# Performance work log

Hardware: AMD Instinct MI355X
Metric: run time of the kernel (lower is better)

Reference implementation:

```python
import jax, jax.numpy as jnp
import numpy as np

LEAKAGE = 0.9
RADIUS = 0.1
AVG_DEGREE = 6


def setup_inputs() -> dict:
    key = jax.random.key(0)
    k1, k2, k3, k4, k5 = jax.random.split(key, 5)
    B, T, I, N, O = 16, 2048, 32, 2048, 32
    input_sequence = jax.random.normal(k1, (B, T, I), dtype=jnp.float32)
    # sparse reservoir matrix, uniform(-1,1) with density avg_degree/N, scaled to spectral radius
    A = jax.random.uniform(k2, (N, N), minval=-1.0, maxval=1.0, dtype=jnp.float32)
    mask = jax.random.uniform(k3, (N, N)) < (AVG_DEGREE / N)
    A = jnp.where(mask, A, 0.0)
    # approximate spectral normalization (power-iteration-free surrogate scale)
    A = A * (RADIUS / jnp.max(jnp.abs(jnp.linalg.eigvals(A))).astype(jnp.float32))
    Win = (RADIUS) * (2.0 * jax.random.uniform(k4, (N, I), dtype=jnp.float32) - 1.0)
    Wout_w = jax.random.normal(k5, (O, N), dtype=jnp.float32) / np.sqrt(N)
    return {"input_sequence": input_sequence, "Win": Win, "A": A, "Wout_w": Wout_w, "washout_len": 64}


def reference(input_sequence, Win, A, Wout_w, washout_len):
    # input projection for all timesteps at once (noise_std = 0.0)
    inp = jnp.einsum('bti,ni->btn', input_sequence, Win)  # [B, T, N]
    B = input_sequence.shape[0]
    N = A.shape[0]
    h0 = jnp.zeros((B, N), dtype=input_sequence.dtype)
    At = A.T

    def step(h, u_t):
        # h: [B, N], u_t: [B, N]
        h_new = (1.0 - LEAKAGE) * h + LEAKAGE * jnp.tanh(h @ At + u_t)
        return h_new, h_new

    _, hs = jax.lax.scan(step, h0, jnp.swapaxes(inp, 0, 1))  # hs: [T, B, N]
    hs = jnp.swapaxes(hs, 0, 1)  # [B, T, N]
    h_list = hs[:, washout_len - 1:]  # keep steps i >= washout_len - 1
    return jnp.einsum('btn,on->bto', h_list, Wout_w)
```

## Files before the change

kernel.cpp:

```cpp
#include <hip/hip_runtime.h>
#include <stdint.h>

#define BB 16
#define TT 2048
#define NI 32
#define NN 2048
#define NO 32
#define WASH 64
#define TO (TT - WASH + 1)
#define W 24
#define WT 24
#define CH 16
#define HBST 2056
#define HBROW 4112
#define UROWB 4132
#define U2OFF 65792
#define LDS_BYTES (U2OFF + CH*UROWB)

typedef short bfvec __attribute__((ext_vector_type(8)));
typedef float f4_t  __attribute__((ext_vector_type(4)));

__device__ inline unsigned short f2bf(float f) {
  unsigned int u = __builtin_bit_cast(unsigned int, f);
  unsigned int r = u + 0x7fffu + ((u >> 16) & 1u);
  return (unsigned short)(r >> 16);
}
__device__ inline float bf2f(unsigned short s) {
  unsigned int u = ((unsigned int)s) << 16;
  return __builtin_bit_cast(float, u);
}
__device__ inline float tanh_fast(float x) {
  x = fminf(15.f, fmaxf(-15.f, x));
  float e = __expf(x + x);
  float r = __builtin_amdgcn_rcpf(e + 1.0f);
  return (e - 1.0f) * r;
}

__global__ void build_ell(const float* __restrict__ A, uint32_t* __restrict__ ell,
                          uint32_t* __restrict__ deg) {
  int gw = (int)((blockIdx.x * blockDim.x + threadIdx.x) >> 6);
  int lane = (int)(threadIdx.x & 63);
  if (gw >= NN) return;
  const float* row = A + (size_t)gw * NN;
  int base = 0;
  for (int c = 0; c < NN; c += 64) {
    float v = row[c + lane];
    bool nz = (v != 0.0f);
    unsigned long long mask = __ballot(nz);
    int pre = __popcll(mask & ((1ull << lane) - 1ull));
    if (nz) {
      int idx = base + pre;
      if (idx < W) {
        uint32_t packed = (((uint32_t)f2bf(v)) << 16) | (uint32_t)((c + lane) * 4);
        ell[(size_t)gw * W + idx] = packed;
      }
    }
    base += __popcll(mask);
  }
  int d = base < W ? base : W;
  if (lane == 0) deg[gw] = (uint32_t)d;
  for (int k = d + lane; k < W; k += 64) ell[(size_t)gw * W + k] = 0u;
}

__global__ void sortperm(const uint32_t* __restrict__ deg, uint32_t* __restrict__ perm,
                         uint32_t* __restrict__ invp) {
  __shared__ int dg[NN];
  int tid = (int)threadIdx.x;
  for (int i = tid; i < NN; i += 256) dg[i] = (int)deg[i];
  __syncthreads();
  int r = (int)blockIdx.x * 256 + tid;
  int d = dg[r];
  int rank = 0;
  for (int j = 0; j < NN; ++j) {
    int dj = dg[j];
    rank += (dj < d) || (dj == d && j < r);
  }
  perm[rank] = (uint32_t)r;
  invp[r] = (uint32_t)rank;
}

__global__ void pairsort(const uint32_t* __restrict__ deg, const uint32_t* __restrict__ perm,
                         uint32_t* __restrict__ pairrank, uint32_t* __restrict__ pp) {
  __shared__ int ps[1024];
  int tid = (int)threadIdx.x;
  for (int i = tid; i < 1024; i += 256) {
    int d0 = (int)deg[perm[i]]; if (d0 > W) d0 = W;
    int d1 = (int)deg[perm[2047 - i]]; if (d1 > W) d1 = W;
    int s = d0 + d1; if (s > WT) s = WT;
    ps[i] = s;
  }
  __syncthreads();
  int p = (int)blockIdx.x * 256 + tid;
  int s = ps[p];
  int rank = 0;
  for (int j = 0; j < 1024; ++j) {
    int sj = ps[j];
    rank += (sj < s) || (sj == s && j < p);
  }
  pairrank[p] = (uint32_t)rank;
  pp[rank] = (uint32_t)p;
}

__device__ inline int rank2pos(int r, const uint32_t* pairrank) {
  return (r < 1024) ? (2 * (int)pairrank[r]) : (2 * (int)pairrank[2047 - r] + 1);
}

__device__ inline int bcnt_get(unsigned long long lo, unsigned long long hi, int b) {
  return (int)(((b < 16) ? (lo >> (4 * b)) : (hi >> (4 * (b - 16)))) & 15ull);
}

__global__ void build_pairs(const uint32_t* __restrict__ ell, const uint32_t* __restrict__ deg,
                            const uint32_t* __restrict__ perm, const uint32_t* __restrict__ invp,
                            const uint32_t* __restrict__ pairrank, const uint32_t* __restrict__ pp,
                            uint32_t* __restrict__ pa, uint32_t* __restrict__ pva,
                            uint32_t* __restrict__ pvb, uint32_t* __restrict__ wavecnt) {
  int blk = (int)blockIdx.x;
  int lane = (int)threadIdx.x;
  int t = blk * 64 + lane;
  int p = (int)pp[t];
  uint32_t a_[WT], u_[WT], w_[WT];
  int cnt = 0;
  {
    int ro = (int)perm[p];
    int d = (int)deg[ro]; if (d > W) d = W;
    for (int k = 0; k < d && cnt < WT; ++k) {
      uint32_t e = ell[(size_t)ro * W + k];
      int pos = rank2pos((int)invp[(e & 0xffffu) >> 2], pairrank);
      a_[cnt] = (uint32_t)(pos * 2);
      u_[cnt] = e & 0xffff0000u;
      w_[cnt] = 0u;
      ++cnt;
    }
    ro = (int)perm[2047 - p];
    d = (int)deg[ro]; if (d > W) d = W;
    for (int k = 0; k < d && cnt < WT; ++k) {
      uint32_t e = ell[(size_t)ro * W + k];
      int pos = rank2pos((int)invp[(e & 0xffffu) >> 2], pairrank);
      a_[cnt] = (uint32_t)(pos * 2);
      u_[cnt] = 0u;
      w_[cnt] = e & 0xffff0000u;
      ++cnt;
    }
  }
  int m = cnt;
  #pragma unroll
  for (int off = 32; off; off >>= 1) m = max(m, __shfl_xor(m, off));
  int S = m < 8 ? 8 : (m > 24 ? 24 : m);
  if (lane == 0) wavecnt[blk] = (uint32_t)S;

  uint32_t sa[WT], su[WT], sw[WT];
  for (int s = 0; s < WT; ++s) {
    sa[s] = ((uint32_t)((lane + s) & 31)) << 2;
    su[s] = 0u; sw[s] = 0u;
  }
  uint32_t used = 0;
  for (int s = 0; s < S; ++s) {
    unsigned long long clo = 0ull, chi = 0ull;
    bool placed = false;
    for (int round = 0; round < 6; ++round) {
      bool force = (round == 5);
      int best = -1, bestc = 999;
      if (!placed) {
        for (int k = 0; k < WT; ++k) {
          if (k >= cnt) break;
          if ((used >> k) & 1u) continue;
        int b = (int)((a_[k] >> 2) & 31u);
          int c = bcnt_get(clo, chi, b);
          if (c < bestc) { bestc = c; best = k; }
        }
      }
      int pb = (!placed && best >= 0) ? (int)((a_[best] >> 2) & 31u) : 32;
      int shift = (s * 19 + round * 7) & 63;
      int mypos = (lane - shift) & 63;
      for (int b = 0; b < 32; ++b) {
        unsigned long long mb = __ballot(pb == b);
        if (!mb) continue;
        unsigned long long mbr = (mb >> shift) | (mb << ((64 - shift) & 63));
        int have = bcnt_get(clo, chi, b);
        int cap = 2 - have; if (cap < 0) cap = 0;
        if (pb == b) {
          int rank = (int)__popcll(mbr & ((1ull << (unsigned)mypos) - 1ull));
          if (force || rank < cap) {
            placed = true;
            used |= (1u << (unsigned)best);
            sa[s] = a_[best]; su[s] = u_[best]; sw[s] = w_[best];
          }
        }
        int nprop = (int)__popcll(mb);
        int add = force ? nprop : (nprop < cap ? nprop : cap);
        int room = 15 - have; if (add > room) add = room;
        if (add > 0) {
          if (b < 16) clo += ((unsigned long long)add) << (4 * b);
          else        chi += ((unsigned long long)add) << (4 * (b - 16));
        }
      }
    }
    if (!placed) {
      int pick = lane & 31;
      for (int j = 0; j < 32; ++j) {
        int b = (lane + j) & 31;
        if (bcnt_get(clo, chi, b) < 2) { pick = b; break; }
      }
      sa[s] = ((uint32_t)pick) << 2;
    }
  }
  for (int k = 0; k < WT; ++k) {
    pa[(size_t)t * WT + k] = sa[k];
    pva[(size_t)t * WT + k] = su[k];
    pvb[(size_t)t * WT + k] = sw[k];
  }
}

__global__ void build_frags(const float* __restrict__ Win, const float* __restrict__ Wout,
                            const uint32_t* __restrict__ perm, const uint32_t* __restrict__ pp,
                            uint32_t* __restrict__ winf, uint32_t* __restrict__ woutf) {
  int f = (int)(blockIdx.x * blockDim.x + threadIdx.x);
  if (f < 32768) {
    int reg = f & 3, lane = (f >> 2) & 63, ntg = f >> 8;
    int n = (ntg << 4) + (lane & 15);
    int k = ((lane >> 4) << 3) + reg * 2;
    int p = (int)pp[n >> 1];
    int np = (int)perm[(n & 1) ? (2047 - p) : p];
    uint32_t lo = f2bf(Win[(size_t)np * NI + k]);
    uint32_t hi = f2bf(Win[(size_t)np * NI + k + 1]);
    winf[f] = lo | (hi << 16);
  } else {
    int g = f - 32768;
    int reg = g & 3, lane = (g >> 2) & 63, kt = (g >> 8) & 63, ot = g >> 14;
    int o = (ot << 4) + (lane & 15);
    int n = (kt << 5) + ((lane >> 4) << 3) + reg * 2;
    int p = (int)pp[n >> 1];
    int n0 = (int)perm[p];
    int n1 = (int)perm[2047 - p];
    uint32_t lo = f2bf(Wout[(size_t)o * NN + n0]);
    uint32_t hi = f2bf(Wout[(size_t)o * NN + n1]);
    woutf[g] = lo | (hi << 16);
  }
}

#define ENT(K, BASE)                                                                 \
  {                                                                                  \
    float hv = bf2f(*(const unsigned short*)(smem + (BASE) + ea##K));                \
    y0 = __builtin_fmaf(__builtin_bit_cast(float, va##K), hv, y0);                   \
    y1 = __builtin_fmaf(__builtin_bit_cast(float, vb##K), hv, y1);                   \
  }

#define ENTS8(B)  ENT(0,B) ENT(1,B) ENT(2,B) ENT(3,B) ENT(4,B) ENT(5,B) ENT(6,B) ENT(7,B)
#define ENTS9(B)  ENTS8(B)  ENT(8,B)
#define ENTS10(B) ENTS9(B)  ENT(9,B)
#define ENTS11(B) ENTS10(B) ENT(10,B)
#define ENTS12(B) ENTS11(B) ENT(11,B)
#define ENTS13(B) ENTS12(B) ENT(12,B)
#define ENTS14(B) ENTS13(B) ENT(13,B)
#define ENTS15(B) ENTS14(B) ENT(14,B)
#define ENTS16(B) ENTS15(B) ENT(15,B)
#define ENTS17(B) ENTS16(B) ENT(16,B)
#define ENTS18(B) ENTS17(B) ENT(17,B)
#define ENTS19(B) ENTS18(B) ENT(18,B)
#define ENTS20(B) ENTS19(B) ENT(19,B)
#define ENTS21(B) ENTS20(B) ENT(20,B)
#define ENTS22(B) ENTS21(B) ENT(21,B)
#define ENTS23(B) ENTS22(B) ENT(22,B)
#define ENTS24(B) ENTS23(B) ENT(23,B)

#define STEPLOOP(ENTS)                                                               \
  _Pragma("unroll 1")                                                                \
  for (int tt = 0; tt < CH; ++tt) {                                                  \
    const int po = ((tt + CH - 1) & (CH - 1)) * HBROW;                               \
    uint32_t uw = *(const uint32_t*)(smem + u2a + tt * UROWB);                       \
    float y0 = bf2f((unsigned short)(uw & 0xffffu));                                 \
    float y1 = bf2f((unsigned short)(uw >> 16));                                     \
    ENTS(po)                                                                         \
    float hn0 = 0.1f * h0 + 0.9f * tanh_fast(y0);                                    \
    float hn1 = 0.1f * h1 + 0.9f * tanh_fast(y1);                                    \
    *(uint32_t*)(smem + hwa + tt * HBROW) =                                          \
        (uint32_t)f2bf(hn0) | ((uint32_t)f2bf(hn1) << 16);                           \
    h0 = hn0; h1 = hn1;                                                              \
    __syncthreads();                                                                 \
  }

__global__ __launch_bounds__(1024, 1) void rec_kernel(
    const float* __restrict__ x,
    const uint32_t* __restrict__ pa, const uint32_t* __restrict__ pva,
    const uint32_t* __restrict__ pvb, const uint32_t* __restrict__ wavecnt,
    const uint32_t* __restrict__ winf, const uint32_t* __restrict__ woutf,
    float* __restrict__ out) {
  extern __shared__ char smem[];
  unsigned short* hb = (unsigned short*)smem;
  float* oscratch = (float*)(smem + U2OFF);

  const int tid = (int)threadIdx.x;
  const int b = (int)blockIdx.x;
  const int lane = tid & 63;
  const int wv = tid >> 6;
  const int la15 = lane & 15;
  const int lg = lane >> 4;
  const int u2a = U2OFF + (tid << 2);
  const int hwa = tid << 2;

  int cnt = __builtin_amdgcn_readfirstlane((int)wavecnt[wv]);

  uint32_t ea0, ea1, ea2, ea3, ea4, ea5, ea6, ea7, ea8, ea9, ea10, ea11,
           ea12, ea13, ea14, ea15, ea16, ea17, ea18, ea19, ea20, ea21, ea22, ea23;
  uint32_t va0, va1, va2, va3, va4, va5, va6, va7, va8, va9, va10, va11,
           va12, va13, va14, va15, va16, va17, va18, va19, va20, va21, va22, va23;
  uint32_t vb0, vb1, vb2, vb3, vb4, vb5, vb6, vb7, vb8, vb9, vb10, vb11,
           vb12, vb13, vb14, vb15, vb16, vb17, vb18, vb19, vb20, vb21, vb22, vb23;
  {
    const uint4* qa = (const uint4*)(pa + (size_t)tid * WT);
    const uint4* qv = (const uint4*)(pva + (size_t)tid * WT);
    const uint4* qw = (const uint4*)(pvb + (size_t)tid * WT);
    uint4 A0 = qa[0], A1 = qa[1], A2 = qa[2], A3 = qa[3], A4 = qa[4], A5 = qa[5];
    uint4 V0 = qv[0], V1 = qv[1], V2 = qv[2], V3 = qv[3], V4 = qv[4], V5 = qv[5];
    uint4 B0 = qw[0], B1 = qw[1], B2 = qw[2], B3 = qw[3], B4 = qw[4], B5 = qw[5];
    ea0 = A0.x; ea1 = A0.y; ea2 = A0.z; ea3 = A0.w;
    ea4 = A1.x; ea5 = A1.y; ea6 = A1.z; ea7 = A1.w;
    ea8 = A2.x; ea9 = A2.y; ea10 = A2.z; ea11 = A2.w;
    ea12 = A3.x; ea13 = A3.y; ea14 = A3.z; ea15 = A3.w;
    ea16 = A4.x; ea17 = A4.y; ea18 = A4.z; ea19 = A4.w;
    ea20 = A5.x; ea21 = A5.y; ea22 = A5.z; ea23 = A5.w;
    va0 = V0.x; va1 = V0.y; va2 = V0.z; va3 = V0.w;
    va4 = V1.x; va5 = V1.y; va6 = V1.z; va7 = V1.w;
    va8 = V2.x; va9 = V2.y; va10 = V2.z; va11 = V2.w;
    va12 = V3.x; va13 = V3.y; va14 = V3.z; va15 = V3.w;
    va16 = V4.x; va17 = V4.y; va18 = V4.z; va19 = V4.w;
    va20 = V5.x; va21 = V5.y; va22 = V5.z; va23 = V5.w;
    vb0 = B0.x; vb1 = B0.y; vb2 = B0.z; vb3 = B0.w;
    vb4 = B1.x; vb5 = B1.y; vb6 = B1.z; vb7 = B1.w;
    vb8 = B2.x; vb9 = B2.y; vb10 = B2.z; vb11 = B2.w;
    vb12 = B3.x; vb13 = B3.y; vb14 = B3.z; vb15 = B3.w;
    vb16 = B4.x; vb17 = B4.y; vb18 = B4.z; vb19 = B4.w;
    vb20 = B5.x; vb21 = B5.y; vb22 = B5.z; vb23 = B5.w;
  }

  *(uint32_t*)(smem + (CH - 1) * HBROW + (tid << 2)) = 0u;
  float h0 = 0.0f, h1 = 0.0f;

  for (int c = 0; c < TT / CH; ++c) {
    const int t0 = c * CH;

    {
      const float* xp = x + ((size_t)b * TT + (t0 + la15)) * NI + (lg << 3);
      float4 x0 = *(const float4*)xp;
      float4 x1 = *(const float4*)(xp + 4);
      union { unsigned short u16[8]; bfvec v; } af;
      af.u16[0]=f2bf(x0.x); af.u16[1]=f2bf(x0.y); af.u16[2]=f2bf(x0.z); af.u16[3]=f2bf(x0.w);
      af.u16[4]=f2bf(x1.x); af.u16[5]=f2bf(x1.y); af.u16[6]=f2bf(x1.z); af.u16[7]=f2bf(x1.w);
      #pragma unroll
      for (int nt = 0; nt < 8; ++nt) {
        int ntg = (wv << 3) + nt;
        union { uint4 q; bfvec v; } bw;
        bw.q = *(const uint4*)(winf + (((size_t)ntg * 64 + lane) << 2));
        f4_t acc = {0.f, 0.f, 0.f, 0.f};
        acc = __builtin_amdgcn_mfma_f32_16x16x32_bf16(bw.v, af.v, acc, 0, 0, 0);
        int dw = (ntg << 3) + (lg << 1);
        uint32_t w0 = (uint32_t)f2bf(acc[0]) | ((uint32_t)f2bf(acc[1]) << 16);
        uint32_t w1 = (uint32_t)f2bf(acc[2]) | ((uint32_t)f2bf(acc[3]) << 16);
        char* ub = smem + U2OFF + la15 * UROWB + (dw << 2);
        *(uint32_t*)(ub) = w0;
        *(uint32_t*)(ub + 4) = w1;
      }
    }
    __syncthreads();

    asm volatile("" : "+s"(cnt));
    if      (cnt <= 8)  { STEPLOOP(ENTS8)  }
    else if (cnt == 9)  { STEPLOOP(ENTS9)  }
    else if (cnt == 10) { STEPLOOP(ENTS10) }
    else if (cnt == 11) { STEPLOOP(ENTS11) }
    else if (cnt == 12) { STEPLOOP(ENTS12) }
    else if (cnt == 13) { STEPLOOP(ENTS13) }
    else if (cnt == 14) { STEPLOOP(ENTS14) }
    else if (cnt == 15) { STEPLOOP(ENTS15) }
    else if (cnt == 16) { STEPLOOP(ENTS16) }
    else if (cnt == 17) { STEPLOOP(ENTS17) }
    else if (cnt == 18) { STEPLOOP(ENTS18) }
    else if (cnt == 19) { STEPLOOP(ENTS19) }
    else if (cnt == 20) { STEPLOOP(ENTS20) }
    else if (cnt == 21) { STEPLOOP(ENTS21) }
    else if (cnt == 22) { STEPLOOP(ENTS22) }
    else if (cnt == 23) { STEPLOOP(ENTS23) }
    else                { STEPLOOP(ENTS24) }

    {
      f4_t oa0 = {0.f,0.f,0.f,0.f}, oa1 = {0.f,0.f,0.f,0.f};
      #pragma unroll
      for (int k4 = 0; k4 < 4; ++k4) {
        int kt = (wv << 2) + k4;
        union { uint4 q; bfvec v; } ha, w0, w1;
        ha.q = *(const uint4*)(hb + (size_t)la15 * HBST + (kt << 5) + (lg << 3));
        w0.q = *(const uint4*)(woutf + (((size_t)(kt) * 64 + lane) << 2));
        w1.q = *(const uint4*)(woutf + (((size_t)(64 + kt) * 64 + lane) << 2));
        oa0 = __builtin_amdgcn_mfma_f32_16x16x32_bf16(ha.v, w0.v, oa0, 0, 0, 0);
        oa1 = __builtin_amdgcn_mfma_f32_16x16x32_bf16(ha.v, w1.v, oa1, 0, 0, 0);
      }
      float* os = oscratch + (wv << 9);
      int tb = lg << 2;
      #pragma unroll
      for (int r = 0; r < 4; ++r) os[(tb + r) * 32 + la15] = oa0[r];
      #pragma unroll
      for (int r = 0; r < 4; ++r) os[(tb + r) * 32 + 16 + la15] = oa1[r];
    }
    __syncthreads();
    if (tid < 512) {
      float s = 0.0f;
      #pragma unroll
      for (int w2 = 0; w2 < 16; ++w2) s += oscratch[(w2 << 9) + tid];
      int tg = t0 + (tid >> 5);
      if (tg >= WASH - 1)
        out[((size_t)b * TO + (tg - (WASH - 1))) * NO + (tid & 31)] = s;
    }
    __syncthreads();
  }
}

extern "C" void kernel_launch(void* const* d_in, const int* in_sizes, int n_in,
                              void* d_out, int out_size, void* d_ws, size_t ws_size,
                              hipStream_t stream) {
  (void)in_sizes; (void)n_in; (void)out_size; (void)ws_size;
  const float* x    = (const float*)d_in[0];
  const float* Win  = (const float*)d_in[1];
  const float* A    = (const float*)d_in[2];
  const float* Wout = (const float*)d_in[3];
  float* out = (float*)d_out;

  char* ws = (char*)d_ws;
  uint32_t* ell      = (uint32_t*)(ws);
  uint32_t* deg      = (uint32_t*)(ws + 196608);
  uint32_t* perm     = (uint32_t*)(ws + 204800);
  uint32_t* invp     = (uint32_t*)(ws + 212992);
  uint32_t* pairrank = (uint32_t*)(ws + 221184);
  uint32_t* pp       = (uint32_t*)(ws + 225280);
  uint32_t* wavecnt  = (uint32_t*)(ws + 229376);
  uint32_t* pa       = (uint32_t*)(ws + 229504);
  uint32_t* pva      = (uint32_t*)(ws + 327808);
  uint32_t* pvb      = (uint32_t*)(ws + 426112);
  uint32_t* winf     = (uint32_t*)(ws + 524416);
  uint32_t* woutf    = (uint32_t*)(ws + 655488);

  hipFuncSetAttribute((const void*)rec_kernel,
                      hipFuncAttributeMaxDynamicSharedMemorySize, 160 * 1024);

  hipLaunchKernelGGL(build_ell, dim3(512), dim3(256), 0, stream, A, ell, deg);
  hipLaunchKernelGGL(sortperm, dim3(8), dim3(256), 0, stream, deg, perm, invp);
  hipLaunchKernelGGL(pairsort, dim3(4), dim3(256), 0, stream, deg, perm, pairrank, pp);
  hipLaunchKernelGGL(build_pairs, dim3(16), dim3(64), 0, stream,
                     ell, deg, perm, invp, pairrank, pp, pa, pva, pvb, wavecnt);
  hipLaunchKernelGGL(build_frags, dim3(256), dim3(256), 0, stream, Win, Wout, perm, pp, winf, woutf);
  hipLaunchKernelGGL(rec_kernel, dim3(16), dim3(1024), LDS_BYTES, stream,
                     x, pa, pva, pvb, wavecnt, winf, woutf, out);
}
```

Measured before the change: 2.858 ms.

## Duplicate hidden state into a swizzled LDS copy to cut bank conflicts

Each step now writes the new hidden state twice: once to the existing history buffer and once to a second, swizzled double-buffered copy. Even-indexed gather entries read from the original layout and odd-indexed ones from the swizzled copy. The host-side slot assignment is rewritten to place one entry per free bank in each half-wave, choosing between the two layouts. This aims to cut LDS bank conflicts in the sparse gather, at the cost of an extra LDS store per step and a larger LDS footprint. The row padding is also removed.

```diff
diff --git a/kernel.cpp b/kernel.cpp
--- a/kernel.cpp
+++ b/kernel.cpp
@@ -11,11 +11,12 @@
 #define W 24
 #define WT 24
 #define CH 16
-#define HBST 2056
-#define HBROW 4112
+#define HBST 2048
+#define HBROW 4096
 #define UROWB 4132
-#define U2OFF 65792
-#define LDS_BYTES (U2OFF + CH*UROWB)
+#define U2OFF 65536
+#define C1OFF 131712
+#define LDS_BYTES (C1OFF + 8192)
 
 typedef short bfvec __attribute__((ext_vector_type(8)));
 typedef float f4_t  __attribute__((ext_vector_type(4)));
@@ -105,8 +106,9 @@
   return (r < 1024) ? (2 * (int)pairrank[r]) : (2 * (int)pairrank[2047 - r] + 1);
 }
 
-__device__ inline int bcnt_get(unsigned long long lo, unsigned long long hi, int b) {
-  return (int)(((b < 16) ? (lo >> (4 * b)) : (hi >> (4 * (b - 16)))) & 15ull);
+__device__ inline int c1pos(int t) {
+  int l = t & 31, h = t >> 5;
+  return (h << 5) | ((17 * l + 5 * h) & 31);
 }
 
 __global__ void build_pairs(const uint32_t* __restrict__ ell, const uint32_t* __restrict__ deg,
@@ -116,9 +118,10 @@
                             uint32_t* __restrict__ pvb, uint32_t* __restrict__ wavecnt) {
   int blk = (int)blockIdx.x;
   int lane = (int)threadIdx.x;
+  int half = lane >> 5;
   int t = blk * 64 + lane;
   int p = (int)pp[t];
-  uint32_t a_[WT], u_[WT], w_[WT];
+  uint32_t a0_[WT], a1_[WT], u_[WT], w_[WT];
   int cnt = 0;
   {
     int ro = (int)perm[p];
@@ -126,7 +129,8 @@
     for (int k = 0; k < d && cnt < WT; ++k) {
       uint32_t e = ell[(size_t)ro * W + k];
       int pos = rank2pos((int)invp[(e & 0xffffu) >> 2], pairrank);
-      a_[cnt] = (uint32_t)(pos * 2);
+      a0_[cnt] = (uint32_t)(pos * 2);
+      a1_[cnt] = (uint32_t)(c1pos(pos >> 1) * 4 + (pos & 1) * 2);
       u_[cnt] = e & 0xffff0000u;
       w_[cnt] = 0u;
       ++cnt;
@@ -136,7 +140,8 @@
     for (int k = 0; k < d && cnt < WT; ++k) {
       uint32_t e = ell[(size_t)ro * W + k];
       int pos = rank2pos((int)invp[(e & 0xffffu) >> 2], pairrank);
-      a_[cnt] = (uint32_t)(pos * 2);
+      a0_[cnt] = (uint32_t)(pos * 2);
+      a1_[cnt] = (uint32_t)(c1pos(pos >> 1) * 4 + (pos & 1) * 2);
       u_[cnt] = 0u;
       w_[cnt] = e & 0xffff0000u;
       ++cnt;
@@ -154,52 +159,64 @@
     su[s] = 0u; sw[s] = 0u;
   }
   uint32_t used = 0;
+  int rem = cnt;
   for (int s = 0; s < S; ++s) {
-    unsigned long long clo = 0ull, chi = 0ull;
+    int copy = s & 1;
+    unsigned long long occ = 0ull;
     bool placed = false;
-    for (int round = 0; round < 6; ++round) {
-      bool force = (round == 5);
-      int best = -1, bestc = 999;
-      if (!placed) {
+    const int R = 4;
+    for (int r = 0; r < R; ++r) {
+      bool last = (r == R - 1);
+      bool urgent = (rem >= S - s);
+      int pk = -1, pb = 32;
+      if (!placed && rem > 0) {
         for (int k = 0; k < WT; ++k) {
           if (k >= cnt) break;
           if ((used >> k) & 1u) continue;
-        int b = (int)((a_[k] >> 2) & 31u);
-          int c = bcnt_get(clo, chi, b);
-          if (c < bestc) { bestc = c; best = k; }
+          int b = copy ? (int)((a1_[k] >> 2) & 31u) : (int)((a0_[k] >> 2) & 31u);
+          if (!((occ >> (half * 32 + b)) & 1ull)) { pk = k; pb = b; break; }
         }
-      }
-      int pb = (!placed && best >= 0) ? (int)((a_[best] >> 2) & 31u) : 32;
-      int shift = (s * 19 + round * 7) & 63;
-      int mypos = (lane - shift) & 63;
+        if (pk < 0 && last && urgent) {
+          for (int k = 0; k < WT; ++k) {
+            if (k >= cnt) break;
+            if (!((used >> k) & 1u)) {
+              pk = k;
+              pb = copy ? (int)((a1_[k] >> 2) & 31u) : (int)((a0_[k] >> 2) & 31u);
+              break;
+            }
+          }
+        }
+      }
+      int shift = (s * 19 + r * 7) & 31;
       for (int b = 0; b < 32; ++b) {
         unsigned long long mb = __ballot(pb == b);
         if (!mb) continue;
-        unsigned long long mbr = (mb >> shift) | (mb << ((64 - shift) & 63));
-        int have = bcnt_get(clo, chi, b);
-        int cap = 2 - have; if (cap < 0) cap = 0;
-        if (pb == b) {
-          int rank = (int)__popcll(mbr & ((1ull << (unsigned)mypos) - 1ull));
-          if (force || rank < cap) {
-            placed = true;
-            used |= (1u << (unsigned)best);
-            sa[s] = a_[best]; su[s] = u_[best]; sw[s] = w_[best];
+        for (int h = 0; h < 2; ++h) {
+          uint32_t mh = (uint32_t)(mb >> (h * 32));
+          if (!mh) continue;
+          bool freeb = !((occ >> (h * 32 + b)) & 1ull);
+          uint32_t mhr = (mh >> shift) | (mh << ((32 - shift) & 31));
+          int winpos = __ffs(mhr) - 1;
+          int winlane = ((winpos + shift) & 31) + h * 32;
+          if (freeb) occ |= 1ull << (h * 32 + b);
+          if (pb == b && half == h && !placed) {
+            bool win = (lane == winlane);
+            if ((freeb && win) || (last && urgent)) {
+              placed = true;
+              used |= 1u << (unsigned)pk;
+              sa[s] = copy ? a1_[pk] : a0_[pk];
+              su[s] = u_[pk]; sw[s] = w_[pk];
+              rem--;
+            }
           }
         }
-        int nprop = (int)__popcll(mb);
-        int add = force ? nprop : (nprop < cap ? nprop : cap);
-        int room = 15 - have; if (add > room) add = room;
-        if (add > 0) {
-          if (b < 16) clo += ((unsigned long long)add) << (4 * b);
-          else        chi += ((unsigned long long)add) << (4 * (b - 16));
-        }
       }
     }
     if (!placed) {
-      int pick = lane & 31;
+      int pick = (lane + s) & 31;
       for (int j = 0; j < 32; ++j) {
-        int b = (lane + j) & 31;
-        if (bcnt_get(clo, chi, b) < 2) { pick = b; break; }
+        int b = (lane + s + j) & 31;
+        if (!((occ >> (half * 32 + b)) & 1ull)) { pick = b; break; }
       }
       sa[s] = ((uint32_t)pick) << 2;
     }
@@ -238,43 +255,45 @@
   }
 }
 
-#define ENT(K, BASE)                                                                 \
+#define ENT(K)                                                                       \
   {                                                                                  \
-    float hv = bf2f(*(const unsigned short*)(smem + (BASE) + ea##K));                \
+    float hv = bf2f(*(const unsigned short*)(smem + ((((K) & 1) ? po1 : po0)) + ea##K)); \
     y0 = __builtin_fmaf(__builtin_bit_cast(float, va##K), hv, y0);                   \
     y1 = __builtin_fmaf(__builtin_bit_cast(float, vb##K), hv, y1);                   \
   }
 
-#define ENTS8(B)  ENT(0,B) ENT(1,B) ENT(2,B) ENT(3,B) ENT(4,B) ENT(5,B) ENT(6,B) ENT(7,B)
-#define ENTS9(B)  ENTS8(B)  ENT(8,B)
-#define ENTS10(B) ENTS9(B)  ENT(9,B)
-#define ENTS11(B) ENTS10(B) ENT(10,B)
-#define ENTS12(B) ENTS11(B) ENT(11,B)
-#define ENTS13(B) ENTS12(B) ENT(12,B)
-#define ENTS14(B) ENTS13(B) ENT(13,B)
-#define ENTS15(B) ENTS14(B) ENT(14,B)
-#define ENTS16(B) ENTS15(B) ENT(15,B)
-#define ENTS17(B) ENTS16(B) ENT(16,B)
-#define ENTS18(B) ENTS17(B) ENT(17,B)
-#define ENTS19(B) ENTS18(B) ENT(18,B)
-#define ENTS20(B) ENTS19(B) ENT(19,B)
-#define ENTS21(B) ENTS20(B) ENT(20,B)
-#define ENTS22(B) ENTS21(B) ENT(21,B)
-#define ENTS23(B) ENTS22(B) ENT(22,B)
-#define ENTS24(B) ENTS23(B) ENT(23,B)
+#define ENTS8  ENT(0) ENT(1) ENT(2) ENT(3) ENT(4) ENT(5) ENT(6) ENT(7)
+#define ENTS9  ENTS8  ENT(8)
+#define ENTS10 ENTS9  ENT(9)
+#define ENTS11 ENTS10 ENT(10)
+#define ENTS12 ENTS11 ENT(11)
+#define ENTS13 ENTS12 ENT(12)
+#define ENTS14 ENTS13 ENT(13)
+#define ENTS15 ENTS14 ENT(14)
+#define ENTS16 ENTS15 ENT(15)
+#define ENTS17 ENTS16 ENT(16)
+#define ENTS18 ENTS17 ENT(17)
+#define ENTS19 ENTS18 ENT(18)
+#define ENTS20 ENTS19 ENT(19)
+#define ENTS21 ENTS20 ENT(20)
+#define ENTS22 ENTS21 ENT(21)
+#define ENTS23 ENTS22 ENT(22)
+#define ENTS24 ENTS23 ENT(23)
 
 #define STEPLOOP(ENTS)                                                               \
   _Pragma("unroll 1")                                                                \
   for (int tt = 0; tt < CH; ++tt) {                                                  \
-    const int po = ((tt + CH - 1) & (CH - 1)) * HBROW;                               \
+    const int po0 = ((tt + CH - 1) & (CH - 1)) << 12;                                \
+    const int po1 = C1OFF + (((tt + 1) & 1) << 12);                                  \
     uint32_t uw = *(const uint32_t*)(smem + u2a + tt * UROWB);                       \
     float y0 = bf2f((unsigned short)(uw & 0xffffu));                                 \
     float y1 = bf2f((unsigned short)(uw >> 16));                                     \
-    ENTS(po)                                                                         \
+    ENTS                                                                             \
     float hn0 = 0.1f * h0 + 0.9f * tanh_fast(y0);                                    \
     float hn1 = 0.1f * h1 + 0.9f * tanh_fast(y1);                                    \
-    *(uint32_t*)(smem + hwa + tt * HBROW) =                                          \
-        (uint32_t)f2bf(hn0) | ((uint32_t)f2bf(hn1) << 16);                           \
+    uint32_t wpk = (uint32_t)f2bf(hn0) | ((uint32_t)f2bf(hn1) << 16);                \
+    *(uint32_t*)(smem + hwa + (tt << 12)) = wpk;                                     \
+    *(uint32_t*)(smem + c1wa + ((tt & 1) << 12)) = wpk;                              \
     h0 = hn0; h1 = hn1;                                                              \
     __syncthreads();                                                                 \
   }
@@ -297,6 +316,7 @@
   const int lg = lane >> 4;
   const int u2a = U2OFF + (tid << 2);
   const int hwa = tid << 2;
+  const int c1wa = C1OFF + (((tid >> 5 << 5) | ((17 * (tid & 31) + 5 * (tid >> 5)) & 31)) << 2);
 
   int cnt = __builtin_amdgcn_readfirstlane((int)wavecnt[wv]);
 
@@ -333,7 +353,8 @@
     vb20 = B5.x; vb21 = B5.y; vb22 = B5.z; vb23 = B5.w;
   }
 
-  *(uint32_t*)(smem + (CH - 1) * HBROW + (tid << 2)) = 0u;
+  *(uint32_t*)(smem + 15 * HBROW + (tid << 2)) = 0u;
+  *(uint32_t*)(smem + C1OFF + 4096 + (tid << 2)) = 0u;
   float h0 = 0.0f, h1 = 0.0f;
 
   for (int c = 0; c < TT / CH; ++c) {
```

Result: slower. 2.931 ms (+2.6%).
